# Kernel tuning notes

Hardware: AMD Instinct MI355X
Metric: run time of the kernel (lower is better)

Reference implementation:

```python
import jax, jax.numpy as jnp
import numpy as np

EMBED_DIM = 1024
HEAD_SIZE = 64
B, T = 8, 2048


def setup_inputs() -> dict:
    key = jax.random.key(0)
    kx, kk, kq, kv = jax.random.split(key, 4)
    s = EMBED_DIM ** -0.5  # linear init scale (arbitrary for baseline)
    return {
        "x": jax.random.normal(kx, (B, T, EMBED_DIM), dtype=jnp.float32),
        "Wk": jax.random.normal(kk, (EMBED_DIM, HEAD_SIZE), dtype=jnp.float32) * s,
        "Wq": jax.random.normal(kq, (EMBED_DIM, HEAD_SIZE), dtype=jnp.float32) * s,
        "Wv": jax.random.normal(kv, (EMBED_DIM, HEAD_SIZE), dtype=jnp.float32) * s,
    }


def reference(x, Wk, Wq, Wv):
    # x: [B, T, C]; projections: [C, H]
    k = jnp.einsum("btc,ch->bth", x, Wk)
    q = jnp.einsum("btc,ch->bth", x, Wq)
    v = jnp.einsum("btc,ch->bth", x, Wv)
    Tlen = x.shape[1]
    scores = jnp.einsum("bqh,bkh->bqk", q, k) * (Wk.shape[1] ** -0.5)  # [B,T,T]
    causal = jnp.tril(jnp.ones((Tlen, Tlen), dtype=bool))
    scores = jnp.where(causal, scores, -jnp.inf)
    weights = jax.nn.softmax(scores, axis=-1)  # dropout=0 (eval mode)
    return jnp.einsum("bqk,bkh->bqh", weights, v)
```

## Files before the change

### kernel.cpp

```cpp
#include <hip/hip_runtime.h>
#include <hip/hip_bf16.h>


typedef __attribute__((ext_vector_type(8))) __bf16 bf16x8;
typedef __attribute__((ext_vector_type(4))) float f32x4;

#define BT   16384
#define TLEN 2048
#define NB   8

__device__ __forceinline__ ushort f2bf(float f) {
    __hip_bfloat16 h = __float2bfloat16(f);
    return __builtin_bit_cast(ushort, h);
}

__global__ void wtrans_kernel(const float* __restrict__ Wk, const float* __restrict__ Wq,
                              const float* __restrict__ Wv, ushort* __restrict__ wtb) {
    int idx = blockIdx.x * 256 + threadIdx.x;
    int e   = idx * 4;
    int s   = e >> 16;
    int rem = e & 65535;
    int k   = rem >> 6;
    int h   = rem & 63;
    const float* W = (s == 0) ? Wk : (s == 1) ? Wq : Wv;
    float sc = (s == 1) ? 0.125f : 1.0f;
    float4 v = *reinterpret_cast<const float4*>(&W[(size_t)k * 64 + h]);
    wtb[(size_t)(s * 64 + h + 0) * 1024 + k] = f2bf(v.x * sc);
    wtb[(size_t)(s * 64 + h + 1) * 1024 + k] = f2bf(v.y * sc);
    wtb[(size_t)(s * 64 + h + 2) * 1024 + k] = f2bf(v.z * sc);
    wtb[(size_t)(s * 64 + h + 3) * 1024 + k] = f2bf(v.w * sc);
}

__global__ __launch_bounds__(256, 4) void qkv_kernel4(
    const float* __restrict__ x, const ushort* __restrict__ wtb,
    ushort* __restrict__ kqv, ushort* __restrict__ vT)
{
    __shared__ __align__(16) f32x4 red[2][12][64];

    const int tid  = threadIdx.x;
    const int lane = tid & 63;
    const int h    = tid >> 6;
    const int m    = lane & 15;
    const int g    = lane >> 4;
    const int R0   = blockIdx.x * 16;

    f32x4 acc[12];
    #pragma unroll
    for (int i = 0; i < 12; ++i) acc[i] = (f32x4){0.f, 0.f, 0.f, 0.f};

    const float*  xp = &x[(size_t)(R0 + m) * 1024 + h * 256 + g * 8];
    const ushort* wb = &wtb[(size_t)m * 1024 + h * 256 + g * 8];

    float4 xa = *reinterpret_cast<const float4*>(xp);
    float4 xb = *reinterpret_cast<const float4*>(xp + 4);

    #pragma unroll
    for (int st = 0; st < 8; ++st) {
        float4 xna, xnb;
        if (st < 7) {
            xna = *reinterpret_cast<const float4*>(xp + (st + 1) * 32);
            xnb = *reinterpret_cast<const float4*>(xp + (st + 1) * 32 + 4);
        }
        union { ushort u[8]; bf16x8 v; } av;
        av.u[0] = f2bf(xa.x); av.u[1] = f2bf(xa.y); av.u[2] = f2bf(xa.z); av.u[3] = f2bf(xa.w);
        av.u[4] = f2bf(xb.x); av.u[5] = f2bf(xb.y); av.u[6] = f2bf(xb.z); av.u[7] = f2bf(xb.w);
        #pragma unroll
        for (int nt = 0; nt < 12; ++nt) {
            bf16x8 b = *reinterpret_cast<const bf16x8*>(wb + (size_t)nt * 16 * 1024 + st * 32);
            acc[nt] = __builtin_amdgcn_mfma_f32_16x16x32_bf16(av.v, b, acc[nt], 0, 0, 0);
        }
        xa = xna; xb = xnb;
    }

    if (h == 1 || h == 3) {
        #pragma unroll
        for (int i = 0; i < 12; ++i) red[h >> 1][i][lane] = acc[i];
    }
    __syncthreads();
    if (h == 0 || h == 2) {
        #pragma unroll
        for (int i = 0; i < 12; ++i) acc[i] += red[h >> 1][i][lane];
    }
    __syncthreads();
    if (h == 2) {
        #pragma unroll
        for (int i = 0; i < 12; ++i) red[0][i][lane] = acc[i];
    }
    __syncthreads();
    if (h == 0) {
        #pragma unroll
        for (int nt = 0; nt < 12; ++nt) {
            f32x4 a = acc[nt] + red[0][nt][lane];
            int s = nt >> 2;
            int c = (nt & 3) * 16 + m;
            #pragma unroll
            for (int j = 0; j < 4; ++j) {
                size_t row = (size_t)R0 + g * 4 + j;
                if (s < 2) kqv[((size_t)s * BT + row) * 64 + c] = f2bf(a[j]);
                else       vT[(size_t)c * BT + row]            = f2bf(a[j]);
            }
        }
    }
}

__global__ __launch_bounds__(256, 3) void attn_kernel3(
    const ushort* __restrict__ qs, const ushort* __restrict__ ks,
    const ushort* __restrict__ vT, float* __restrict__ out)
{
    __shared__ __align__(16) ushort kt[2][64][80];
    __shared__ __align__(16) ushort vt[2][64][80];
    __shared__ __align__(16) ushort pl[4][16][72];

    const int bid = blockIdx.x;
    const int i   = 63 - (bid >> 3);
    const int b   = bid & 7;
    const int Ti  = (i >> 1) + 1;

    const int tid  = threadIdx.x;
    const int lane = tid & 63;
    const int wv   = tid >> 6;
    const int wq   = wv & 1;
    const int hf   = wv >> 1;
    const int m    = lane & 15;
    const int g    = lane >> 4;
    const int ko   = g * 8;
    const int rowb = g * 4;
    const size_t base = (size_t)b * TLEN;
    const int qr0 = i * 32 + wq * 16;

    bf16x8 qa[2];
    {
        size_t row_g = base + qr0 + m;
        qa[0] = *reinterpret_cast<const bf16x8*>(&qs[row_g * 64 + 0 + ko]);
        qa[1] = *reinterpret_cast<const bf16x8*>(&qs[row_g * 64 + 32 + ko]);
    }

    f32x4 o[4];
    #pragma unroll
    for (int nt = 0; nt < 4; ++nt) o[nt] = (f32x4){0.f, 0.f, 0.f, 0.f};
    float mrun[4] = {-1e30f, -1e30f, -1e30f, -1e30f};
    float lrun[4] = {0.f, 0.f, 0.f, 0.f};

    const int hs2 = tid >> 7;
    const int tl  = tid & 127;
    const int sr  = tl >> 1;
    const int sh  = (tl & 1) * 32;

    const int nit = (Ti + 1) >> 1;
    for (int it = 0; it < nit; ++it) {
        int ts = 2 * it + hs2;
        if (ts < Ti) {
            const ushort* ksrc = &ks[(base + (size_t)ts * 64 + sr) * 64 + sh];
            uint4* kdst = reinterpret_cast<uint4*>(&kt[hs2][sr][sh]);
            #pragma unroll
            for (int q = 0; q < 4; ++q) kdst[q] = reinterpret_cast<const uint4*>(ksrc)[q];
            const ushort* vsrc = &vT[(size_t)sr * BT + base + (size_t)ts * 64 + sh];
            uint4* vdst = reinterpret_cast<uint4*>(&vt[hs2][sr][sh]);
            #pragma unroll
            for (int q = 0; q < 4; ++q) vdst[q] = reinterpret_cast<const uint4*>(vsrc)[q];
        }
        __syncthreads();

        int t = 2 * it + hf;
        if (t < Ti) {
            f32x4 s[4];
            #pragma unroll
            for (int nt = 0; nt < 4; ++nt) s[nt] = (f32x4){0.f, 0.f, 0.f, 0.f};
            #pragma unroll
            for (int kk = 0; kk < 2; ++kk) {
                #pragma unroll
                for (int nt = 0; nt < 4; ++nt) {
                    bf16x8 bb = *reinterpret_cast<const bf16x8*>(&kt[hf][nt * 16 + m][kk * 32 + ko]);
                    s[nt] = __builtin_amdgcn_mfma_f32_16x16x32_bf16(qa[kk], bb, s[nt], 0, 0, 0);
                }
            }
            if (t == Ti - 1) {
                #pragma unroll
                for (int nt = 0; nt < 4; ++nt)
                    #pragma unroll
                    for (int j = 0; j < 4; ++j)
                        if (t * 64 + nt * 16 + m > qr0 + rowb + j) s[nt][j] = -1e30f;
            }
            #pragma unroll
            for (int j = 0; j < 4; ++j) {
                float mx = fmaxf(fmaxf(s[0][j], s[1][j]), fmaxf(s[2][j], s[3][j]));
                #pragma unroll
                for (int d = 1; d < 16; d <<= 1) mx = fmaxf(mx, __shfl_xor(mx, d, 64));
                float mnew = fmaxf(mrun[j], mx);
                float corr = __expf(mrun[j] - mnew);
                mrun[j] = mnew;
                float p0 = __expf(s[0][j] - mnew);
                float p1 = __expf(s[1][j] - mnew);
                float p2 = __expf(s[2][j] - mnew);
                float p3 = __expf(s[3][j] - mnew);
                float ps = p0 + p1 + p2 + p3;
                #pragma unroll
                for (int d = 1; d < 16; d <<= 1) ps += __shfl_xor(ps, d, 64);
                lrun[j] = lrun[j] * corr + ps;
                #pragma unroll
                for (int nt = 0; nt < 4; ++nt) o[nt][j] *= corr;
                pl[wv][rowb + j][0 * 16 + m] = f2bf(p0);
                pl[wv][rowb + j][1 * 16 + m] = f2bf(p1);
                pl[wv][rowb + j][2 * 16 + m] = f2bf(p2);
                pl[wv][rowb + j][3 * 16 + m] = f2bf(p3);
            }
            asm volatile("s_waitcnt lgkmcnt(0)" ::: "memory");
            __builtin_amdgcn_sched_barrier(0);
            #pragma unroll
            for (int kk = 0; kk < 2; ++kk) {
                bf16x8 pa = *reinterpret_cast<const bf16x8*>(&pl[wv][m][kk * 32 + ko]);
                #pragma unroll
                for (int nt = 0; nt < 4; ++nt) {
                    bf16x8 vb = *reinterpret_cast<const bf16x8*>(&vt[hf][nt * 16 + m][kk * 32 + ko]);
                    o[nt] = __builtin_amdgcn_mfma_f32_16x16x32_bf16(pa, vb, o[nt], 0, 0, 0);
                }
            }
        }
        __syncthreads();
    }

    float* mg = reinterpret_cast<float*>(&kt[0][0][0]);
    float* st = reinterpret_cast<float*>(&vt[0][0][0]);
    if (hf == 1) {
        #pragma unroll
        for (int nt = 0; nt < 4; ++nt)
            *reinterpret_cast<f32x4*>(&mg[((wq * 4 + nt) * 64 + lane) * 4]) = o[nt];
        if (m == 0) {
            #pragma unroll
            for (int j = 0; j < 4; ++j) {
                st[(wq * 16 + rowb + j) * 2 + 0] = mrun[j];
                st[(wq * 16 + rowb + j) * 2 + 1] = lrun[j];
            }
        }
    }
    __syncthreads();
    if (hf == 0) {
        float ea[4], eb[4], li[4];
        #pragma unroll
        for (int j = 0; j < 4; ++j) {
            float m1 = st[(wq * 16 + rowb + j) * 2 + 0];
            float l1 = st[(wq * 16 + rowb + j) * 2 + 1];
            float mm = fmaxf(mrun[j], m1);
            ea[j] = __expf(mrun[j] - mm);
            eb[j] = __expf(m1 - mm);
            li[j] = 1.0f / (lrun[j] * ea[j] + l1 * eb[j]);
        }
        #pragma unroll
        for (int nt = 0; nt < 4; ++nt) {
            f32x4 ob = *reinterpret_cast<const f32x4*>(&mg[((wq * 4 + nt) * 64 + lane) * 4]);
            #pragma unroll
            for (int j = 0; j < 4; ++j) {
                size_t rrow = base + qr0 + rowb + j;
                out[rrow * 64 + nt * 16 + m] = (o[nt][j] * ea[j] + ob[j] * eb[j]) * li[j];
            }
        }
    }
}

extern "C" void kernel_launch(void* const* d_in, const int* in_sizes, int n_in,
                              void* d_out, int out_size, void* d_ws, size_t ws_size,
                              hipStream_t stream) {
    const float* x  = (const float*)d_in[0];
    const float* Wk = (const float*)d_in[1];
    const float* Wq = (const float*)d_in[2];
    const float* Wv = (const float*)d_in[3];
    float* out = (float*)d_out;

    ushort* ws   = (ushort*)d_ws;
    ushort* kqv  = ws;
    ushort* kbuf = ws;
    ushort* qbuf = ws + (size_t)BT * 64;
    ushort* vTb  = ws + (size_t)2 * BT * 64;
    ushort* wtb  = ws + (size_t)3 * BT * 64;

    wtrans_kernel<<<dim3(192), 256, 0, stream>>>(Wk, Wq, Wv, wtb);
    qkv_kernel4<<<dim3(1024), 256, 0, stream>>>(x, wtb, kqv, vTb);
    attn_kernel3<<<dim3(512), 256, 0, stream>>>(qbuf, kbuf, vTb, out);
}
```

Baseline: 176.5 us.

## Restructure QKV projection into LDS double-buffered tiled GEMM over 32-row blocks

The QKV projection kernel is rewritten as a classic tiled GEMM. Each block handles 32 rows and stages x (converted to bf16) and the transposed weights into swizzled, double-buffered shared memory. Waves now split the output columns instead of the K dimension, which removes the cross-wave reduction through LDS, and each weight tile loaded from global memory is reused across 32 rows instead of 16. The cost is more shared memory (about 56 KB), a lower occupancy target, and two barriers per K step.

```diff
diff --git a/kernel.cpp b/kernel.cpp
--- a/kernel.cpp
+++ b/kernel.cpp
@@ -31,76 +31,99 @@
     wtb[(size_t)(s * 64 + h + 3) * 1024 + k] = f2bf(v.w * sc);
 }
 
-__global__ __launch_bounds__(256, 4) void qkv_kernel4(
+__global__ __launch_bounds__(256, 2) void qkv_kernel5(
     const float* __restrict__ x, const ushort* __restrict__ wtb,
-    ushort* __restrict__ kqv, ushort* __restrict__ vT)
+    ushort* __restrict__ kq, ushort* __restrict__ vT)
 {
-    __shared__ __align__(16) f32x4 red[2][12][64];
+    __shared__ __align__(16) ushort xs[2][32 * 64];
+    __shared__ __align__(16) ushort bs[2][192 * 64];
 
     const int tid  = threadIdx.x;
     const int lane = tid & 63;
-    const int h    = tid >> 6;
+    const int wv   = tid >> 6;
+    const int r    = wv & 1;
+    const int ch   = wv >> 1;
     const int m    = lane & 15;
     const int g    = lane >> 4;
-    const int R0   = blockIdx.x * 16;
-
-    f32x4 acc[12];
+    const int R0   = blockIdx.x * 32;
+
+    f32x4 acc[6];
     #pragma unroll
-    for (int i = 0; i < 12; ++i) acc[i] = (f32x4){0.f, 0.f, 0.f, 0.f};
-
-    const float*  xp = &x[(size_t)(R0 + m) * 1024 + h * 256 + g * 8];
-    const ushort* wb = &wtb[(size_t)m * 1024 + h * 256 + g * 8];
-
-    float4 xa = *reinterpret_cast<const float4*>(xp);
-    float4 xb = *reinterpret_cast<const float4*>(xp + 4);
+    for (int i = 0; i < 6; ++i) acc[i] = (f32x4){0.f, 0.f, 0.f, 0.f};
+
+    float4 xr[2];
+    uint4  br[6];
+
+#define LOADX(kt)                                                                   \
+    _Pragma("unroll")                                                               \
+    for (int i = 0; i < 2; ++i) {                                                   \
+        int id = i * 256 + tid, rX = id >> 4, c4 = id & 15;                         \
+        xr[i] = *reinterpret_cast<const float4*>(                                   \
+            &x[(size_t)(R0 + rX) * 1024 + (kt) * 64 + c4 * 4]);                     \
+    }
+#define LOADB(kt)                                                                   \
+    _Pragma("unroll")                                                               \
+    for (int i = 0; i < 6; ++i) {                                                   \
+        int id = i * 256 + tid, nB = id >> 3, cb = id & 7;                          \
+        br[i] = *reinterpret_cast<const uint4*>(                                    \
+            &wtb[(size_t)nB * 1024 + (kt) * 64 + cb * 8]);                          \
+    }
+#define WRITE(buf)                                                                  \
+    _Pragma("unroll")                                                               \
+    for (int i = 0; i < 2; ++i) {                                                   \
+        int id = i * 256 + tid, rX = id >> 4, c4 = id & 15;                         \
+        int ph = (c4 >> 1) ^ (rX & 7);                                              \
+        ushort4 u;                                                                  \
+        u.x = f2bf(xr[i].x); u.y = f2bf(xr[i].y);                                   \
+        u.z = f2bf(xr[i].z); u.w = f2bf(xr[i].w);                                   \
+        *reinterpret_cast<ushort4*>(&xs[buf][rX * 64 + ph * 8 + (c4 & 1) * 4]) = u; \
+    }                                                                               \
+    _Pragma("unroll")                                                               \
+    for (int i = 0; i < 6; ++i) {                                                   \
+        int id = i * 256 + tid, nB = id >> 3, cb = id & 7;                          \
+        int ph = cb ^ (nB & 7);                                                     \
+        *reinterpret_cast<uint4*>(&bs[buf][nB * 64 + ph * 8]) = br[i];              \
+    }
+
+    LOADX(0); LOADB(0);
+    WRITE(0);
+    __syncthreads();
+
+    for (int kt = 0; kt < 16; ++kt) {
+        const int cur = kt & 1;
+        if (kt < 15) { LOADX(kt + 1); LOADB(kt + 1); }
+        #pragma unroll
+        for (int kk = 0; kk < 2; ++kk) {
+            int pc = (4 * kk + g) ^ (m & 7);
+            bf16x8 a = *reinterpret_cast<const bf16x8*>(&xs[cur][(r * 16 + m) * 64 + pc * 8]);
+            #pragma unroll
+            for (int nt = 0; nt < 6; ++nt) {
+                int n = ch * 96 + nt * 16 + m;
+                bf16x8 b = *reinterpret_cast<const bf16x8*>(&bs[cur][n * 64 + pc * 8]);
+                acc[nt] = __builtin_amdgcn_mfma_f32_16x16x32_bf16(a, b, acc[nt], 0, 0, 0);
+            }
+        }
+        __syncthreads();
+        if (kt < 15) {
+            WRITE(cur ^ 1);
+            __syncthreads();
+        }
+    }
 
     #pragma unroll
-    for (int st = 0; st < 8; ++st) {
-        float4 xna, xnb;
-        if (st < 7) {
-            xna = *reinterpret_cast<const float4*>(xp + (st + 1) * 32);
-            xnb = *reinterpret_cast<const float4*>(xp + (st + 1) * 32 + 4);
-        }
-        union { ushort u[8]; bf16x8 v; } av;
-        av.u[0] = f2bf(xa.x); av.u[1] = f2bf(xa.y); av.u[2] = f2bf(xa.z); av.u[3] = f2bf(xa.w);
-        av.u[4] = f2bf(xb.x); av.u[5] = f2bf(xb.y); av.u[6] = f2bf(xb.z); av.u[7] = f2bf(xb.w);
-        #pragma unroll
-        for (int nt = 0; nt < 12; ++nt) {
-            bf16x8 b = *reinterpret_cast<const bf16x8*>(wb + (size_t)nt * 16 * 1024 + st * 32);
-            acc[nt] = __builtin_amdgcn_mfma_f32_16x16x32_bf16(av.v, b, acc[nt], 0, 0, 0);
-        }
-        xa = xna; xb = xnb;
-    }
-
-    if (h == 1 || h == 3) {
-        #pragma unroll
-        for (int i = 0; i < 12; ++i) red[h >> 1][i][lane] = acc[i];
-    }
-    __syncthreads();
-    if (h == 0 || h == 2) {
-        #pragma unroll
-        for (int i = 0; i < 12; ++i) acc[i] += red[h >> 1][i][lane];
-    }
-    __syncthreads();
-    if (h == 2) {
-        #pragma unroll
-        for (int i = 0; i < 12; ++i) red[0][i][lane] = acc[i];
-    }
-    __syncthreads();
-    if (h == 0) {
-        #pragma unroll
-        for (int nt = 0; nt < 12; ++nt) {
-            f32x4 a = acc[nt] + red[0][nt][lane];
-            int s = nt >> 2;
-            int c = (nt & 3) * 16 + m;
-            #pragma unroll
-            for (int j = 0; j < 4; ++j) {
-                size_t row = (size_t)R0 + g * 4 + j;
-                if (s < 2) kqv[((size_t)s * BT + row) * 64 + c] = f2bf(a[j]);
-                else       vT[(size_t)c * BT + row]            = f2bf(a[j]);
-            }
-        }
-    }
+    for (int nt = 0; nt < 6; ++nt) {
+        int c = ch * 96 + nt * 16 + m;
+        #pragma unroll
+        for (int j = 0; j < 4; ++j) {
+            size_t row = (size_t)R0 + r * 16 + g * 4 + j;
+            ushort v = f2bf(acc[nt][j]);
+            if (c < 128) kq[((size_t)(c >> 6) * BT + row) * 64 + (c & 63)] = v;
+            else         vT[(size_t)(c - 128) * BT + row] = v;
+        }
+    }
+#undef LOADX
+#undef LOADB
+#undef WRITE
 }
 
 __global__ __launch_bounds__(256, 3) void attn_kernel3(
@@ -267,13 +290,13 @@
     float* out = (float*)d_out;
 
     ushort* ws   = (ushort*)d_ws;
-    ushort* kqv  = ws;
+    ushort* kq   = ws;
     ushort* kbuf = ws;
     ushort* qbuf = ws + (size_t)BT * 64;
     ushort* vTb  = ws + (size_t)2 * BT * 64;
     ushort* wtb  = ws + (size_t)3 * BT * 64;
 
     wtrans_kernel<<<dim3(192), 256, 0, stream>>>(Wk, Wq, Wv, wtb);
-    qkv_kernel4<<<dim3(1024), 256, 0, stream>>>(x, wtb, kqv, vTb);
+    qkv_kernel5<<<dim3(512), 256, 0, stream>>>(x, wtb, kq, vTb);
     attn_kernel3<<<dim3(512), 256, 0, stream>>>(qbuf, kbuf, vTb, out);
 }
```

After: 158.0 us. 10.5% less time.
